# Kernel tuning notes

Hardware: AMD Instinct MI355X
Metric: run time of the kernel (lower is better)

The kernel has to match this reference:

```python
import jax, jax.numpy as jnp
import numpy as np

B, N, H, HEADS = 4, 2048, 1024, 16
D = H // HEADS  # head dim = 64

def rotate_half(x):
    x1, x2 = jnp.split(x, 2, axis=-1)
    return jnp.concatenate((-x2, x1), axis=-1)

def apply_rope(pos, t):
    # pos: [n, d] broadcasts against t: [b, h, n, d]
    return t * jnp.cos(pos) + rotate_half(t) * jnp.sin(pos)

def setup_inputs() -> dict:
    key = jax.random.key(0)
    k1, k2, k3, k4 = jax.random.split(key, 4)
    x = jax.random.normal(k1, (B, N, H), dtype=jnp.float32)
    rotary_emb = jax.random.normal(k2, (N, D), dtype=jnp.float32)
    # torch Linear(H, 3H, bias=False): weight [3H, H], y = x @ W.T
    w_qkv = jax.random.normal(k3, (3 * H, H), dtype=jnp.float32) * (1.0 / np.sqrt(H))
    w_out = jax.random.normal(k4, (H, H), dtype=jnp.float32) * (1.0 / np.sqrt(H))
    return {"x": x, "rotary_emb": rotary_emb, "w_qkv": w_qkv, "w_out": w_out}

def reference(x, rotary_emb, w_qkv, w_out):
    qkv = jnp.einsum('bnh,oh->bno', x, w_qkv)  # [B, N, 3H]
    q, k, v = jnp.split(qkv, 3, axis=-1)
    def split_heads(t):
        return t.reshape(B, N, HEADS, D).transpose(0, 2, 1, 3)  # b h n d
    q, k, v = map(split_heads, (q, k, v))
    q = apply_rope(rotary_emb, q)
    k = apply_rope(rotary_emb, k)
    scale = 1.0 / np.sqrt(D).astype(np.float32)
    scores = jnp.einsum('bhqd,bhkd->bhqk', q, k) * scale
    attn = jax.nn.softmax(scores, axis=-1)
    out = jnp.einsum('bhqk,bhkd->bhqd', attn, v)
    out = out.transpose(0, 2, 1, 3).reshape(B, N, H)  # b n (h d)
    return jnp.einsum('bnh,oh->bno', out, w_out)
```

## Files before the change

### kernel.cpp

```cpp
#include <hip/hip_runtime.h>
#include <hip/hip_fp16.h>
#include <stdint.h>

#define DEVI __device__ __forceinline__

using f16x2 = __attribute__((ext_vector_type(2))) _Float16;
using f16x8 = __attribute__((ext_vector_type(8))) _Float16;
using f32x4 = __attribute__((ext_vector_type(4))) float;
using f32x16 = __attribute__((ext_vector_type(16))) float;
using u32x4 = __attribute__((ext_vector_type(4))) uint32_t;

DEVI void gload_lds16(const void* g, void* lds) {
  using GP = const __attribute__((address_space(1))) void*;
  using LP = __attribute__((address_space(3))) void*;
  __builtin_amdgcn_global_load_lds((GP)g, (LP)lds, 16, 0, 0);
}

DEVI uint32_t pack2h(float a, float b) {
  return (uint32_t)__half_as_ushort(__float2half(a)) |
         ((uint32_t)__half_as_ushort(__float2half(b)) << 16);
}

DEVI uint32_t cvtpk(float a, float b) {
  auto h2 = __builtin_amdgcn_cvt_pkrtz(a, b);
  return __builtin_bit_cast(uint32_t, h2);
}

DEVI void plswap(uint32_t& a, uint32_t& b) {
  asm volatile("v_permlane32_swap_b32 %0, %1" : "+v"(a), "+v"(b));
}

DEVI float dot2acc(uint32_t w, f16x2 one, float c) {
  return __builtin_amdgcn_fdot2(__builtin_bit_cast(f16x2, w), one, c, false);
}

DEVI float fmax3(float a, float b, float c) { return fmaxf(fmaxf(a, b), c); }

__global__ __launch_bounds__(256) void cvt3_f32_f16(const float* __restrict__ x,
                                                    const float* __restrict__ wq,
                                                    const float* __restrict__ wo,
                                                    __half* __restrict__ xb,
                                                    __half* __restrict__ wqb,
                                                    __half* __restrict__ wob) {
  int i = blockIdx.x * 256 + threadIdx.x;
  const float* in;
  __half* out;
  int j;
  if (i < 1048576) {
    in = x; out = xb; j = i;
  } else if (i < 1048576 + 393216) {
    in = wq; out = wqb; j = i - 1048576;
  } else {
    in = wo; out = wob; j = i - 1441792;
  }
  float4 a = ((const float4*)in)[j * 2];
  float4 b = ((const float4*)in)[j * 2 + 1];
  uint4 u;
  u.x = pack2h(a.x, a.y);
  u.y = pack2h(a.z, a.w);
  u.z = pack2h(b.x, b.y);
  u.w = pack2h(b.z, b.w);
  ((uint4*)out)[j] = u;
}

#define GEMM_CORE(A_, B_, K_, BX_, BY_)                                                 \
  __shared__ __half As[128 * 64];                                                       \
  __shared__ __half Bs[128 * 64];                                                       \
  const int tid = threadIdx.x;                                                          \
  const int w = tid >> 6, l = tid & 63;                                                 \
  const int wm = w >> 1, wn = w & 1;                                                    \
  const int m16 = l & 15, g = l >> 4;                                                   \
  const int row0 = (BY_)*128, col0 = (BX_)*128;                                         \
  const int srow = l >> 3;                                                              \
  const int ks = ((l & 7) ^ srow) * 8;                                                  \
  f32x4 acc[4][4] = {};                                                                 \
  for (int kt = 0; kt < (K_); kt += 64) {                                               \
    __syncthreads();                                                                    \
    _Pragma("unroll") for (int i = 0; i < 4; ++i) {                                     \
      int c = w * 4 + i;                                                                \
      int r = c * 8 + srow;                                                             \
      gload_lds16((A_) + (size_t)(row0 + r) * (K_) + kt + ks, (char*)As + c * 1024);    \
      gload_lds16((B_) + (size_t)(col0 + r) * (K_) + kt + ks, (char*)Bs + c * 1024);    \
    }                                                                                   \
    __syncthreads();                                                                    \
    _Pragma("unroll") for (int kk = 0; kk < 2; ++kk) {                                  \
      f16x8 aF[4], bF[4];                                                               \
      _Pragma("unroll") for (int mi = 0; mi < 4; ++mi) {                                \
        int r = wm * 64 + mi * 16 + m16;                                                \
        aF[mi] = *(const f16x8*)((const char*)As + r * 128 + (((kk * 4 + g) ^ (r & 7)) << 4)); \
      }                                                                                 \
      _Pragma("unroll") for (int ni = 0; ni < 4; ++ni) {                                \
        int r = wn * 64 + ni * 16 + m16;                                                \
        bF[ni] = *(const f16x8*)((const char*)Bs + r * 128 + (((kk * 4 + g) ^ (r & 7)) << 4)); \
      }                                                                                 \
      _Pragma("unroll") for (int mi = 0; mi < 4; ++mi)                                  \
          _Pragma("unroll") for (int ni = 0; ni < 4; ++ni)                              \
              acc[mi][ni] = __builtin_amdgcn_mfma_f32_16x16x32_f16(aF[mi], bF[ni],      \
                                                                   acc[mi][ni], 0, 0, 0); \
    }                                                                                   \
  }

__global__ __launch_bounds__(256) void gemm_qkv_rope(const __half* __restrict__ A,
                                                     const __half* __restrict__ B,
                                                     const float* __restrict__ rot,
                                                     __half* __restrict__ qr,
                                                     __half* __restrict__ kr,
                                                     __half* __restrict__ vr) {
  const int id = blockIdx.y * 24 + blockIdx.x;
  const int nid = (id & 7) * 192 + (id >> 3);
  const int bx = nid % 24, by = nid / 24;

  GEMM_CORE(A, B, 1024, bx, by)

  const int s = bx >> 3;
  const int hh = (bx & 7) * 2 + wn;
  if (s < 2) {
    const float sc = (s == 0) ? 0.18033688011112042f : 1.0f;
    __half* base = (s == 0) ? qr : kr;
#pragma unroll
    for (int mi = 0; mi < 4; ++mi)
#pragma unroll
      for (int j = 0; j < 4; ++j) {
        int r = row0 + wm * 64 + mi * 16 + g * 4 + j;
        int n = r & 2047;
        int bh = (r >> 11) * 16 + hh;
        __half* orow = base + ((size_t)bh * 2048 + n) * 64;
        const float* rp = rot + n * 64;
#pragma unroll
        for (int ni = 0; ni < 2; ++ni) {
          int dlo = ni * 16 + m16;
          float xlo = acc[mi][ni][j], xhi = acc[mi][ni + 2][j];
          float s0, c0, s1, c1;
          __sincosf(rp[dlo], &s0, &c0);
          __sincosf(rp[dlo + 32], &s1, &c1);
          orow[dlo]      = __float2half((xlo * c0 - xhi * s0) * sc);
          orow[dlo + 32] = __float2half((xhi * c1 + xlo * s1) * sc);
        }
      }
  } else {
#pragma unroll
    for (int mi = 0; mi < 4; ++mi)
#pragma unroll
      for (int j = 0; j < 4; ++j) {
        int r = row0 + wm * 64 + mi * 16 + g * 4 + j;
        int n = r & 2047;
        int bh = (r >> 11) * 16 + hh;
        __half* vcol = vr + ((size_t)bh * 64) * 2048 + n;
#pragma unroll
        for (int ni = 0; ni < 4; ++ni) {
          int d = ni * 16 + m16;
          vcol[(size_t)d * 2048] = __float2half(acc[mi][ni][j]);
        }
      }
  }
}

__global__ __launch_bounds__(256) void gemm_bt_f32(const __half* __restrict__ A,
                                                   const __half* __restrict__ B,
                                                   float* __restrict__ C, int N, int K) {
  const int id = blockIdx.y * 8 + blockIdx.x;
  const int nid = (id & 7) * 64 + (id >> 3);
  const int bx = nid % 8, by = nid / 8;

  GEMM_CORE(A, B, K, bx, by)
#pragma unroll
  for (int mi = 0; mi < 4; ++mi)
#pragma unroll
    for (int ni = 0; ni < 4; ++ni)
#pragma unroll
      for (int j = 0; j < 4; ++j) {
        int r = row0 + wm * 64 + mi * 16 + g * 4 + j;
        int cc = col0 + wn * 64 + ni * 16 + m16;
        C[(size_t)r * N + cc] = acc[mi][ni][j];
      }
}

__global__ __launch_bounds__(256, 4) void attn_fwd(const __half* __restrict__ qr,
                                                   const __half* __restrict__ kr,
                                                   const __half* __restrict__ vr,
                                                   __half* __restrict__ out) {
  __shared__ __half K2[2 * 64 * 64];
  __shared__ __half V2[2 * 64 * 64];

  int bid = blockIdx.x;
  bid = (bid & 7) * 128 + (bid >> 3);
  const int bh = bid >> 4;
  const int q0 = (bid & 15) * 128;
  const int tid = threadIdx.x;
  const int w = tid >> 6, l = tid & 63;
  const int q = l & 31, hi = l >> 5;
  const size_t headoff = (size_t)bh * 2048 * 64;

  f16x8 qB[4];
  {
    const __half* qp = qr + headoff + (size_t)(q0 + w * 32 + q) * 64 + hi * 8;
#pragma unroll
    for (int c = 0; c < 4; ++c) qB[c] = *(const f16x8*)(qp + c * 16);
  }

  int kf[4];
#pragma unroll
  for (int c = 0; c < 4; ++c)
    kf[c] = q * 128 + 16 * (hi ^ (q & 1)) + 32 * (c ^ ((q >> 1) & 3));
  const int vbase = q * 128 + ((hi ^ (q & 7)) << 4);

  const int krow_l = l >> 3, kslot = l & 7;
  const __half* kb = kr + headoff;
  const __half* vb = vr + (size_t)bh * 64 * 2048;

  auto STAGE = [&](int buf, int kv0) {
#pragma unroll
    for (int i = 0; i < 2; ++i) {
      int c = w * 2 + i;
      int row = c * 8 + krow_l;
      gload_lds16(kb + (size_t)(kv0 + row) * 64 + ((kslot ^ (row & 7)) * 8),
                  (char*)K2 + buf * 8192 + c * 1024);
    }
#pragma unroll
    for (int i = 0; i < 2; ++i) {
      int c = w * 2 + i;
      int d = c * 8 + (l >> 3);
      gload_lds16(vb + (size_t)d * 2048 + kv0 + (((l & 7) ^ (l >> 3)) * 8),
                  (char*)V2 + buf * 8192 + c * 1024);
    }
  };

  const f16x2 one2 = {(_Float16)1.f, (_Float16)1.f};
  f32x16 o0 = {}, o1 = {};
  float mreg = -1e30f, lreg = 0.f;

  STAGE(0, 0);
  __syncthreads();

  for (int t = 0; t < 32; ++t) {
    const int buf = t & 1;
    if (t < 31) STAGE(buf ^ 1, (t + 1) * 64);

    const char* Kb = (const char*)K2 + buf * 8192;
    const char* Vb = (const char*)V2 + buf * 8192;
#pragma unroll
    for (int kvb = 0; kvb < 2; ++kvb) {
      f32x16 s = {};
      __builtin_amdgcn_s_setprio(1);
#pragma unroll
      for (int c = 0; c < 4; ++c) {
        f16x8 kA = *(const f16x8*)(Kb + kvb * 4096 + kf[c]);
        s = __builtin_amdgcn_mfma_f32_32x32x16_f16(kA, qB[c], s, 0, 0, 0);
      }
      __builtin_amdgcn_s_setprio(0);

      float mt = fmax3(s[0], s[1], s[2]);
      mt = fmax3(mt, s[3], s[4]);
      mt = fmax3(mt, s[5], s[6]);
      mt = fmax3(mt, s[7], s[8]);
      mt = fmax3(mt, s[9], s[10]);
      mt = fmax3(mt, s[11], s[12]);
      mt = fmax3(mt, s[13], s[14]);
      mt = fmaxf(mt, s[15]);
      mt = fmaxf(mt, __shfl_xor(mt, 32));
      if (__any(mt - mreg > 8.f)) {
        float mnew = fmaxf(mreg, mt);
        float alpha = __builtin_amdgcn_exp2f(mreg - mnew);
        lreg *= alpha;
        o0 *= alpha;
        o1 *= alpha;
        mreg = mnew;
      }
      uint32_t W[8];
      float rs = 0.f;
#pragma unroll
      for (int i2 = 0; i2 < 8; ++i2) {
        float e0 = __builtin_amdgcn_exp2f(s[2 * i2] - mreg);
        float e1 = __builtin_amdgcn_exp2f(s[2 * i2 + 1] - mreg);
        W[i2] = cvtpk(e0, e1);
        rs = dot2acc(W[i2], one2, rs);
      }
      rs += __shfl_xor(rs, 32);
      lreg += rs;

      plswap(W[0], W[2]);
      plswap(W[1], W[3]);
      plswap(W[4], W[6]);
      plswap(W[5], W[7]);
      u32x4 f0 = {W[0], W[1], W[2], W[3]};
      u32x4 f1 = {W[4], W[5], W[6], W[7]};
      f16x8 pA0 = __builtin_bit_cast(f16x8, f0);
      f16x8 pA1 = __builtin_bit_cast(f16x8, f1);

      const int vx = vbase ^ (kvb << 6);
      const int vx2 = vx ^ 32;
      f16x8 v00 = *(const f16x8*)(Vb + vx);
      f16x8 v01 = *(const f16x8*)(Vb + vx + 4096);
      f16x8 v10 = *(const f16x8*)(Vb + vx2);
      f16x8 v11 = *(const f16x8*)(Vb + vx2 + 4096);
      __builtin_amdgcn_s_setprio(1);
      o0 = __builtin_amdgcn_mfma_f32_32x32x16_f16(pA0, v00, o0, 0, 0, 0);
      o1 = __builtin_amdgcn_mfma_f32_32x32x16_f16(pA0, v01, o1, 0, 0, 0);
      o0 = __builtin_amdgcn_mfma_f32_32x32x16_f16(pA1, v10, o0, 0, 0, 0);
      o1 = __builtin_amdgcn_mfma_f32_32x32x16_f16(pA1, v11, o1, 0, 0, 0);
      __builtin_amdgcn_s_setprio(0);
    }

    __syncthreads();
  }

  const int b = bh >> 4, hh = bh & 15;
  float invl = 1.0f / lreg;
#pragma unroll
  for (int r = 0; r < 16; ++r) {
    int qrow = (r & 3) + 8 * (r >> 2) + 4 * hi;
    float inv = __shfl(invl, qrow);
    __half* orow = out + (size_t)(b * 2048 + q0 + w * 32 + qrow) * 1024 + hh * 64;
    orow[q] = __float2half(o0[r] * inv);
    orow[32 + q] = __float2half(o1[r] * inv);
  }
}

extern "C" void kernel_launch(void* const* d_in, const int* in_sizes, int n_in,
                              void* d_out, int out_size, void* d_ws, size_t ws_size,
                              hipStream_t stream) {
  const float* x    = (const float*)d_in[0];
  const float* rot  = (const float*)d_in[1];
  const float* wqkv = (const float*)d_in[2];
  const float* wout = (const float*)d_in[3];
  float* out = (float*)d_out;
  char* ws = (char*)d_ws;

  __half* xb    = (__half*)(ws + 0);
  __half* wqkvb = (__half*)(ws + (16ull << 20));
  __half* woutb = (__half*)(ws + (22ull << 20));
  __half* qr    = (__half*)(ws + (24ull << 20));
  __half* ao    = (__half*)(ws + (40ull << 20));
  __half* kr    = (__half*)(ws + (72ull << 20));
  __half* vr    = (__half*)(ws + (88ull << 20));

  cvt3_f32_f16<<<6144, 256, 0, stream>>>(x, wqkv, wout, xb, wqkvb, woutb);
  gemm_qkv_rope<<<dim3(24, 64), 256, 0, stream>>>(xb, wqkvb, rot, qr, kr, vr);
  attn_fwd<<<1024, 256, 0, stream>>>(qr, kr, vr, ao);
  gemm_bt_f32<<<dim3(8, 64), 256, 0, stream>>>(ao, woutb, out, 1024, 1024);
}
```

Baseline: 212.3 us.

## Enlarge QKV GEMM tile to 256x128 with 512-thread blocks

```diff
diff --git a/kernel.cpp b/kernel.cpp
--- a/kernel.cpp
+++ b/kernel.cpp
@@ -100,17 +100,62 @@
     }                                                                                   \
   }
 
-__global__ __launch_bounds__(256) void gemm_qkv_rope(const __half* __restrict__ A,
-                                                     const __half* __restrict__ B,
-                                                     const float* __restrict__ rot,
-                                                     __half* __restrict__ qr,
-                                                     __half* __restrict__ kr,
-                                                     __half* __restrict__ vr) {
+__global__ __launch_bounds__(512, 4) void gemm_qkv_rope(const __half* __restrict__ A,
+                                                        const __half* __restrict__ B,
+                                                        const float* __restrict__ rot,
+                                                        __half* __restrict__ qr,
+                                                        __half* __restrict__ kr,
+                                                        __half* __restrict__ vr) {
+  __shared__ __half As[256 * 64];
+  __shared__ __half Bs[128 * 64];
+  const int tid = threadIdx.x;
+  const int w = tid >> 6, l = tid & 63;
+  const int wm = w >> 1, wn = w & 1;
+  const int m16 = l & 15, g = l >> 4;
   const int id = blockIdx.y * 24 + blockIdx.x;
-  const int nid = (id & 7) * 192 + (id >> 3);
+  const int nid = (id & 7) * 96 + (id >> 3);
   const int bx = nid % 24, by = nid / 24;
-
-  GEMM_CORE(A, B, 1024, bx, by)
+  const int row0 = by * 256, col0 = bx * 128;
+  const int srow = l >> 3;
+  const int ks = ((l & 7) ^ srow) * 8;
+
+  f32x4 acc[4][4] = {};
+
+  for (int kt = 0; kt < 1024; kt += 64) {
+    __syncthreads();
+#pragma unroll
+    for (int i = 0; i < 4; ++i) {
+      int c = w * 4 + i;
+      int r = c * 8 + srow;
+      gload_lds16(A + (size_t)(row0 + r) * 1024 + kt + ks, (char*)As + c * 1024);
+    }
+#pragma unroll
+    for (int i = 0; i < 2; ++i) {
+      int c = w * 2 + i;
+      int r = c * 8 + srow;
+      gload_lds16(B + (size_t)(col0 + r) * 1024 + kt + ks, (char*)Bs + c * 1024);
+    }
+    __syncthreads();
+#pragma unroll
+    for (int kk = 0; kk < 2; ++kk) {
+      f16x8 aF[4], bF[4];
+#pragma unroll
+      for (int mi = 0; mi < 4; ++mi) {
+        int r = wm * 64 + mi * 16 + m16;
+        aF[mi] = *(const f16x8*)((const char*)As + r * 128 + (((kk * 4 + g) ^ (r & 7)) << 4));
+      }
+#pragma unroll
+      for (int ni = 0; ni < 4; ++ni) {
+        int r = wn * 64 + ni * 16 + m16;
+        bF[ni] = *(const f16x8*)((const char*)Bs + r * 128 + (((kk * 4 + g) ^ (r & 7)) << 4));
+      }
+#pragma unroll
+      for (int mi = 0; mi < 4; ++mi)
+#pragma unroll
+        for (int ni = 0; ni < 4; ++ni)
+          acc[mi][ni] = __builtin_amdgcn_mfma_f32_16x16x32_f16(aF[mi], bF[ni], acc[mi][ni], 0, 0, 0);
+    }
+  }
 
   const int s = bx >> 3;
   const int hh = (bx & 7) * 2 + wn;
@@ -335,7 +380,7 @@
   __half* vr    = (__half*)(ws + (88ull << 20));
 
   cvt3_f32_f16<<<6144, 256, 0, stream>>>(x, wqkv, wout, xb, wqkvb, woutb);
-  gemm_qkv_rope<<<dim3(24, 64), 256, 0, stream>>>(xb, wqkvb, rot, qr, kr, vr);
+  gemm_qkv_rope<<<dim3(24, 32), 512, 0, stream>>>(xb, wqkvb, rot, qr, kr, vr);
   attn_fwd<<<1024, 256, 0, stream>>>(qr, kr, vr, ao);
   gemm_bt_f32<<<dim3(8, 64), 256, 0, stream>>>(ao, woutb, out, 1024, 1024);
 }
```

After: 227.3 us. 1.07x slower.
